# Performance work log

Measured on AMD Instinct MI355X. Metric: run time of the kernel, lower is better.

The kernel has to match this reference:

```python
import jax, jax.numpy as jnp
import numpy as np

N, CIN, COUT, K = 16384, 3, 3, 20

def prelu(x, a):
    return jnp.maximum(x, 0) + a * jnp.minimum(x, 0)

def knn_ind(x, k):
    # pairwise squared distances; topk of -d includes self (d=0), matching torch
    xx = jnp.sum(x * x, axis=1, keepdims=True)          # [n,1]
    d = xx + xx.T - 2.0 * (x @ x.T)                      # [n,n]
    return jax.lax.top_k(-d, k)[1]                       # [n,k] int32

def graph_features(x, k):
    ind = knn_ind(x, k)                                  # [n,k]
    xi = x[ind]                                          # [n,k,C] gather
    x_ = jnp.broadcast_to(x[:, None, :], xi.shape)       # [n,k,C]
    return jnp.concatenate([xi - x_, x_], axis=-1)       # [n,k,2C]

def edge_conv(x, k, layers):
    f = graph_features(x, k)                             # [n,k,2C]
    for (W, a) in layers:
        f = prelu(f @ W, a)
    return jnp.max(f, axis=-2)                           # [n,Cout] max over k neighbors

def setup_inputs() -> dict:
    key = jax.random.key(0)
    ks = jax.random.split(key, 16)
    def w(kk, i, o):
        return jax.random.normal(kk, (i, o), jnp.float32) * (1.0 / np.sqrt(i))
    p = jnp.float32(0.25)
    return {
        "x": jax.random.normal(ks[0], (N, CIN), jnp.float32),
        "hidden": jax.random.normal(ks[1], (1,), jnp.float32),
        "W1a": w(ks[2], 2 * CIN, 64), "p1a": p,
        "W1b": w(ks[3], 64, 64),      "p1b": p,
        "W2a": w(ks[4], 128, 64),     "p2a": p,
        "W2b": w(ks[5], 64, 64),      "p2b": p,
        "W3":  w(ks[6], 128, 64),     "p3": p,
        "W4":  w(ks[7], 192, 1024),   "p4": p,
        "W5":  w(ks[8], 1024 + 192, 256), "p5": p,
        "W6":  w(ks[9], 256, 256),    "p6": p,
        "W7":  w(ks[10], 256, 128),   "p7": p,
        "W8":  w(ks[11], 128, COUT),  "p8": p,
    }

def reference(x, hidden, W1a, p1a, W1b, p1b, W2a, p2a, W2b, p2b, W3, p3,
              W4, p4, W5, p5, W6, p6, W7, p7, W8, p8):
    n = x.shape[0]
    x1 = edge_conv(x, K, [(W1a, p1a), (W1b, p1b)])       # [n,64]
    x2 = edge_conv(x1, K, [(W2a, p2a), (W2b, p2b)])      # [n,64]
    x3 = edge_conv(x2, K, [(W3, p3)])                    # [n,64]
    x4 = jnp.concatenate([x1, x2, x3], axis=-1)          # [n,192]
    x5 = prelu(x4 @ W4, p4)                              # [n,1024]
    x5 = jnp.broadcast_to(jnp.max(x5, axis=0, keepdims=True), (n, 1024))
    h = jnp.concatenate([x1, x2, x3, x5], axis=-1)       # [n,1216]
    h = prelu(h @ W5, p5)                                # dropout = identity (eval)
    h = prelu(h @ W6, p6)
    h = prelu(h @ W7, p7)
    h = prelu(h @ W8, p8)                                # [n,COUT]
    return (h, hidden)
```

## Files before the change

kernel.cpp:

```cpp
#include <hip/hip_runtime.h>
#include <hip/hip_bf16.h>
#include <float.h>

#define NPTS 16384
#define KK 20
#define COUT 3
#define SURV_CAP 256
#define RQSLOTS 256

typedef float f4 __attribute__((ext_vector_type(4)));
typedef float f32x4 __attribute__((ext_vector_type(4)));
typedef short bh8 __attribute__((ext_vector_type(8)));

__device__ __forceinline__ void ins20(float (&td)[KK], float &kmax, float nd) {
  float cd = nd;
#pragma unroll
  for (int j = 0; j < KK; ++j) {
    float t0 = td[j];
    bool lt = cd < t0;
    td[j] = lt ? cd : t0;
    cd = lt ? t0 : cd;
  }
  kmax = td[KK - 1];
}

__device__ __forceinline__ void ins4(float (&td)[4], float &kmax, float nd) {
  float cd = nd;
#pragma unroll
  for (int j = 0; j < 4; ++j) {
    float t0 = td[j];
    bool lt = cd < t0;
    td[j] = lt ? cd : t0;
    cd = lt ? t0 : cd;
  }
  kmax = td[3];
}

__device__ __forceinline__ void ins20p(float (&td)[KK], int (&ti)[KK],
                                       float &kmax, float nd, int ni) {
  float cd = nd; int ci = ni;
#pragma unroll
  for (int j = 0; j < KK; ++j) {
    float t0 = td[j]; int t1 = ti[j];
    bool lt = cd < t0;
    td[j] = lt ? cd : t0;  ti[j] = lt ? ci : t1;
    cd = lt ? t0 : cd;     ci = lt ? t1 : ci;
  }
  kmax = td[KK - 1];
}

template<int C>
__global__ void norms_kernel(const float* __restrict__ X, int ldx, float* __restrict__ vn) {
  int i = blockIdx.x * 256 + threadIdx.x;
  if (i >= NPTS) return;
  const float* row = X + (size_t)i * ldx;
  float s = 0.f;
#pragma unroll
  for (int c = 0; c < C; ++c) s = fmaf(row[c], row[c], s);
  vn[i] = s;
}

__global__ __launch_bounds__(256)
void mean64_kernel(const float* __restrict__ X, int ldx, float* __restrict__ mean) {
  __shared__ float p[256];
  const int d = blockIdx.x, t = threadIdx.x;
  float s = 0.f;
  for (int r = t; r < NPTS; r += 256) s += X[(size_t)r * ldx + d];
  p[t] = s;
  __syncthreads();
  for (int o = 128; o > 0; o >>= 1) { if (t < o) p[t] += p[t + o]; __syncthreads(); }
  if (t == 0) mean[d] = p[0] * (1.0f / NPTS);
}

__global__ __launch_bounds__(256)
void xc_kernel(const float* __restrict__ X, int ldx, const float* __restrict__ mean,
               float* __restrict__ Xc, short* __restrict__ Xbf,
               float* __restrict__ vn, float* __restrict__ sn) {
  __shared__ float msh[64];
  const int t = threadIdx.x;
  if (t < 64) msh[t] = mean[t];
  __syncthreads();
  const int row = blockIdx.x * 32 + (t >> 3), sub = t & 7;
  f4 a = *(const f4*)&X[(size_t)row * ldx + sub * 8];
  f4 b = *(const f4*)&X[(size_t)row * ldx + sub * 8 + 4];
#pragma unroll
  for (int e = 0; e < 4; ++e) { a[e] -= msh[sub * 8 + e]; b[e] -= msh[sub * 8 + 4 + e]; }
  *(f4*)&Xc[(size_t)row * 64 + sub * 8] = a;
  *(f4*)&Xc[(size_t)row * 64 + sub * 8 + 4] = b;
  bh8 o;
#pragma unroll
  for (int e = 0; e < 4; ++e) {
    __hip_bfloat16 ha = __float2bfloat16(a[e]);
    __hip_bfloat16 hb = __float2bfloat16(b[e]);
    o[e] = *reinterpret_cast<short*>(&ha);
    o[4 + e] = *reinterpret_cast<short*>(&hb);
  }
  *(bh8*)&Xbf[(size_t)row * 64 + sub * 8] = o;
  float s = a[0]*a[0] + a[1]*a[1] + a[2]*a[2] + a[3]*a[3]
          + b[0]*b[0] + b[1]*b[1] + b[2]*b[2] + b[3]*b[3];
  s += __shfl_xor(s, 1);
  s += __shfl_xor(s, 2);
  s += __shfl_xor(s, 4);
  if (sub == 0) { vn[row] = s; sn[row] = sqrtf(s); }
}

template<int C>
__global__ __launch_bounds__(256, 2)
void sampleTv4_kernel(const float* __restrict__ X, const float* __restrict__ vn,
                      float* __restrict__ plist) {
  __shared__ __align__(16) float Qs[C * 64];
  __shared__ __align__(16) float Cs[C * 132];
  __shared__ float cn[128];
  const int t = threadIdx.x;
  const int qb = blockIdx.x * 64;
  const int tb = blockIdx.y ? 11 : 0;
  const int nt = blockIdx.y ? 10 : 11;

  if constexpr (C == 64) {
#pragma unroll
    for (int u = 0; u < 4; ++u) {
      int idx = u * 256 + t;
      int q = idx & 63, dg = idx >> 6;
      f4 v = *(const f4*)&X[(size_t)(qb + q) * C + dg * 4];
#pragma unroll
      for (int e = 0; e < 4; ++e) Qs[(dg * 4 + e) * 64 + q] = v[e];
    }
  } else {
    for (int idx = t; idx < C * 64; idx += 256) {
      int q = idx & 63, d = idx >> 6;
      Qs[d * 64 + q] = X[(size_t)(qb + q) * C + d];
    }
  }

  const int tq = t & 15, tc = t >> 4;
  const int q0 = tq * 4, c0 = tc * 8;

  float l4[4][4]; float km[4];
#pragma unroll
  for (int i = 0; i < 4; ++i) {
    km[i] = FLT_MAX;
#pragma unroll
    for (int k = 0; k < 4; ++k) l4[i][k] = FLT_MAX;
  }

  for (int tt = 0; tt < nt; ++tt) {
    const int base = (tb + tt) * 128;
    __syncthreads();
    if constexpr (C == 64) {
#pragma unroll
      for (int u = 0; u < 8; ++u) {
        int idx = u * 256 + t;
        int r = idx & 127, dg = idx >> 7;
        f4 v = *(const f4*)&X[(size_t)((base + r) * 6) * C + dg * 4];
#pragma unroll
        for (int e = 0; e < 4; ++e) Cs[(dg * 4 + e) * 132 + r] = v[e];
      }
    } else {
      for (int idx = t; idx < C * 128; idx += 256) {
        int r = idx & 127, d = idx >> 7;
        Cs[d * 132 + r] = X[(size_t)((base + r) * 6) * C + d];
      }
    }
    if (t < 128) cn[t] = vn[(base + t) * 6];
    __syncthreads();

    float acc[4][8];
#pragma unroll
    for (int i = 0; i < 4; ++i)
#pragma unroll
      for (int j = 0; j < 8; ++j) acc[i][j] = 0.f;

#pragma unroll 4
    for (int d = 0; d < C; ++d) {
      f4 qa = *(const f4*)&Qs[d * 64 + q0];
      f4 ca = *(const f4*)&Cs[d * 132 + c0];
      f4 cb = *(const f4*)&Cs[d * 132 + c0 + 4];
      float cr[8] = {ca[0], ca[1], ca[2], ca[3], cb[0], cb[1], cb[2], cb[3]};
#pragma unroll
      for (int i = 0; i < 4; ++i)
#pragma unroll
        for (int j = 0; j < 8; ++j)
          acc[i][j] = fmaf(qa[i], cr[j], acc[i][j]);
    }

#pragma unroll
    for (int j = 0; j < 8; ++j) {
      float cv = cn[c0 + j];
#pragma unroll
      for (int i = 0; i < 4; ++i) {
        float sv = fmaf(-2.f, acc[i][j], cv);
        if (sv < km[i]) ins4(l4[i], km[i], sv);
      }
    }
  }

#pragma unroll
  for (int i = 0; i < 4; ++i) {
    size_t off = (((size_t)blockIdx.y * NPTS + (qb + q0 + i)) * 16 + tc) * 4;
    f4 v = {l4[i][0], l4[i][1], l4[i][2], l4[i][3]};
    *(f4*)&plist[off] = v;
  }
}

__global__ __launch_bounds__(256)
void mergeT_kernel(const float* __restrict__ plist, float* __restrict__ T,
                   unsigned* __restrict__ cnt, unsigned* __restrict__ redoCnt) {
  const int q = blockIdx.x * 256 + threadIdx.x;
  float td[KK];
#pragma unroll
  for (int j = 0; j < KK; ++j) td[j] = FLT_MAX;
  float km = FLT_MAX;
  for (int s = 0; s < 2; ++s) {
    const float* p = &plist[((size_t)s * NPTS + q) * 64];
    for (int z = 0; z < 64; ++z) {
      float v = p[z];
      if (v < km) ins20(td, km, v);
    }
  }
  T[q] = td[KK - 1] + 1e-4f * (fabsf(td[KK - 1]) + 1.0f);
  cnt[q] = 0u;
  if (q == 0) *redoCnt = 0u;
}

__global__ __launch_bounds__(256, 2)
void knn_filter3_kernel(const float* __restrict__ X, const float* __restrict__ vn,
                        const float* __restrict__ T,
                        float* __restrict__ survd, int* __restrict__ survi,
                        unsigned* __restrict__ cnt) {
  constexpr int CAPB = 40;
  __shared__ __align__(16) f4 CsV[512];
  __shared__ float Tsl[128];
  __shared__ unsigned scnt[128];
  __shared__ float sbD[128 * CAPB];
  __shared__ int   sbI[128 * CAPB];

  const int t = threadIdx.x;
  const int qb = blockIdx.x * 128;
  const int cbase = blockIdx.y * 2048;
  if (t < 128) { Tsl[t] = T[qb + t]; scnt[t] = 0u; }
  __syncthreads();

  const int tq = t & 15, tc = t >> 4;
  const int q0 = tq * 8, c0loc = tc * 8;

  float qx[8], qy[8], qz[8], tr[8];
#pragma unroll
  for (int i = 0; i < 8; ++i) {
    const float* qr = &X[(size_t)(qb + q0 + i) * 3];
    qx[i] = qr[0]; qy[i] = qr[1]; qz[i] = qr[2];
    tr[i] = Tsl[q0 + i];
  }

  for (int rd = 0; rd < 4; ++rd) {
    const int cb = cbase + rd * 512;
    __syncthreads();
#pragma unroll
    for (int u = 0; u < 2; ++u) {
      int idx = u * 256 + t;
      int c = cb + idx;
      const float* cr = &X[(size_t)c * 3];
      f4 v = {cr[0], cr[1], cr[2], vn[c]};
      CsV[idx] = v;
    }
    __syncthreads();

#pragma unroll
    for (int sub = 0; sub < 4; ++sub) {
      const int cl0 = sub * 128 + c0loc;
#pragma unroll
      for (int j = 0; j < 8; ++j) {
        f4 cv = CsV[cl0 + j];
        const int cglob = cb + cl0 + j;
#pragma unroll
        for (int i = 0; i < 8; ++i) {
          float d0 = fmaf(qx[i], cv[0], fmaf(qy[i], cv[1], qz[i] * cv[2]));
          float sv = fmaf(-2.f, d0, cv[3]);
          if (sv <= tr[i]) {
            unsigned p = atomicAdd(&scnt[q0 + i], 1u);
            if (p < CAPB) {
              sbD[(q0 + i) * CAPB + p] = sv;
              sbI[(q0 + i) * CAPB + p] = cglob;
            } else {
              unsigned gp = atomicAdd(&cnt[qb + q0 + i], 1u);
              if (gp < SURV_CAP) {
                survd[(size_t)(qb + q0 + i) * SURV_CAP + gp] = sv;
                survi[(size_t)(qb + q0 + i) * SURV_CAP + gp] = cglob;
              }
            }
          }
        }
      }
    }
  }

  __syncthreads();
  if (t < 128) {
    unsigned n = scnt[t]; if (n > CAPB) n = CAPB;
    if (n) {
      unsigned base = atomicAdd(&cnt[qb + t], n);
      for (unsigned i = 0; i < n; ++i) {
        unsigned p = base + i;
        if (p < SURV_CAP) {
          survd[(size_t)(qb + t) * SURV_CAP + p] = sbD[t * CAPB + i];
          survi[(size_t)(qb + t) * SURV_CAP + p] = sbI[t * CAPB + i];
        }
      }
    }
  }
}

__global__ __launch_bounds__(256, 2)
void knn_filter64_mfma(const short* __restrict__ Xbf, const float* __restrict__ vn,
                       const float* __restrict__ sn, const float* __restrict__ T,
                       int* __restrict__ survi, unsigned* __restrict__ cnt) {
  __shared__ __align__(16) short Qs[128 * 64];
  __shared__ __align__(16) short Cs[128 * 64];
  __shared__ float vnc[128], snq[128], snc[128], Tq[128];
  __shared__ unsigned scnt[128];
  __shared__ int sbI[128 * 8];

  const int t = threadIdx.x;
  const int qb = blockIdx.x * 128, cb = blockIdx.y * 128;

#pragma unroll
  for (int p = 0; p < 4; ++p) {
    int idx = p * 256 + t;
    int row = idx >> 3, sl = idx & 7;
    int slq = sl ^ (row & 7);
    *(bh8*)&Qs[row * 64 + slq * 8] = *(const bh8*)&Xbf[(size_t)(qb + row) * 64 + sl * 8];
    *(bh8*)&Cs[row * 64 + slq * 8] = *(const bh8*)&Xbf[(size_t)(cb + row) * 64 + sl * 8];
  }
  if (t < 128) { Tq[t] = T[qb + t]; snq[t] = sn[qb + t]; scnt[t] = 0u; }
  else { vnc[t - 128] = vn[cb + t - 128]; snc[t - 128] = sn[cb + t - 128]; }
  __syncthreads();

  const int w = t >> 6, l = t & 63;
  const int qsub = (w >> 1) * 64, csub = (w & 1) * 64;
  const int lr = l & 15, lh = l >> 4;

  f32x4 acc[4][4];
#pragma unroll
  for (int i = 0; i < 4; ++i)
#pragma unroll
    for (int j = 0; j < 4; ++j) acc[i][j] = f32x4{0.f, 0.f, 0.f, 0.f};

#pragma unroll
  for (int kk = 0; kk < 2; ++kk) {
    const int sl = kk * 4 + lh;
    bh8 af[4], bf[4];
#pragma unroll
    for (int i = 0; i < 4; ++i) {
      int qr = qsub + i * 16 + lr;
      af[i] = *(const bh8*)&Qs[qr * 64 + (sl ^ (qr & 7)) * 8];
      int cr = csub + i * 16 + lr;
      bf[i] = *(const bh8*)&Cs[cr * 64 + (sl ^ (cr & 7)) * 8];
    }
#pragma unroll
    for (int i = 0; i < 4; ++i)
#pragma unroll
      for (int j = 0; j < 4; ++j)
        acc[i][j] = __builtin_amdgcn_mfma_f32_16x16x32_bf16(af[i], bf[j], acc[i][j], 0, 0, 0);
  }

#pragma unroll
  for (int i = 0; i < 4; ++i) {
#pragma unroll
    for (int r = 0; r < 4; ++r) {
      const int ql = qsub + i * 16 + lh * 4 + r;
      const float tcut = Tq[ql];
      const float sq = snq[ql];
      const int q = qb + ql;
#pragma unroll
      for (int j = 0; j < 4; ++j) {
        const int cl = csub + j * 16 + lr;
        float s = fmaf(-2.f, acc[i][j][r], vnc[cl]);
        float margin = 0.0082f * sq * snc[cl] + 1e-6f;
        if (s <= tcut + margin) {
          unsigned p = atomicAdd(&scnt[ql], 1u);
          if (p < 8u) sbI[ql * 8 + p] = cb + cl;
          else {
            unsigned gp = atomicAdd(&cnt[q], 1u);
            if (gp < SURV_CAP) survi[(size_t)q * SURV_CAP + gp] = cb + cl;
          }
        }
      }
    }
  }

  __syncthreads();
  if (t < 128) {
    unsigned n = scnt[t]; if (n > 8u) n = 8u;
    if (n) {
      unsigned base = atomicAdd(&cnt[qb + t], n);
      for (unsigned i = 0; i < n; ++i) {
        unsigned p = base + i;
        if (p < SURV_CAP) survi[(size_t)(qb + t) * SURV_CAP + p] = sbI[t * 8 + i];
      }
    }
  }
}

template<int C>
__global__ __launch_bounds__(256, 2)
void exact_kernel(const float* __restrict__ X, int ldx, const float* __restrict__ vn,
                  const unsigned* __restrict__ cnt, const int* __restrict__ survi,
                  float* __restrict__ survd) {
  __shared__ float qsh[C];
  const int q = blockIdx.x;
  const int t = threadIdx.x;
  if (t < C) qsh[t] = X[(size_t)q * ldx + t];
  __syncthreads();
  unsigned n = cnt[q];
  if (n > SURV_CAP) n = SURV_CAP;
  if (t < n) {
    const int c = survi[(size_t)q * SURV_CAP + t];
    const float* crow = X + (size_t)c * ldx;
    float d0 = 0.f, d1 = 0.f, d2 = 0.f, d3 = 0.f;
#pragma unroll
    for (int s = 0; s < C / 4; ++s) {
      f4 cv = *(const f4*)&crow[s * 4];
      d0 = fmaf(cv[0], qsh[s * 4 + 0], d0);
      d1 = fmaf(cv[1], qsh[s * 4 + 1], d1);
      d2 = fmaf(cv[2], qsh[s * 4 + 2], d2);
      d3 = fmaf(cv[3], qsh[s * 4 + 3], d3);
    }
    survd[(size_t)q * SURV_CAP + t] = fmaf(-2.f, (d0 + d1) + (d2 + d3), vn[c]);
  }
}

__global__ __launch_bounds__(256, 2)
void select_kernel(const float* __restrict__ survd, const int* __restrict__ survi,
                   const unsigned* __restrict__ cnt, int* __restrict__ ind,
                   unsigned* __restrict__ redoCnt, int* __restrict__ redoList) {
  const int q = blockIdx.x * 256 + threadIdx.x;
  const unsigned n = cnt[q];
  if (n > SURV_CAP) {
    unsigned p = atomicAdd(redoCnt, 1u);
    redoList[p] = q;
    return;
  }
  float td[KK]; int ti[KK];
#pragma unroll
  for (int j = 0; j < KK; ++j) { td[j] = FLT_MAX; ti[j] = 0; }
  float kmax = FLT_MAX;
  for (unsigned i = 0; i < n; ++i) {
    float d = survd[(size_t)q * SURV_CAP + i];
    if (d < kmax) ins20p(td, ti, kmax, d, survi[(size_t)q * SURV_CAP + i]);
  }
#pragma unroll
  for (int j = 0; j < KK; ++j) ind[q * KK + j] = ti[j];
}

template<int C>
__global__ __launch_bounds__(256, 2)
void knn_redo_p1(const float* __restrict__ X, int ldx, const float* __restrict__ vn,
                 const int* __restrict__ redoList, const unsigned* __restrict__ redoCnt,
                 float* __restrict__ rpd, int* __restrict__ rpi) {
  __shared__ float lds_d[256 * KK];
  __shared__ int   lds_i[256 * KK];
  const int t = threadIdx.x;
  const unsigned n = *redoCnt;
  const unsigned e = blockIdx.x >> 5;
  const int part = blockIdx.x & 31;
  if (e >= n || e >= (unsigned)RQSLOTS) return;
  const int q = redoList[e];
  float qreg[C];
#pragma unroll
  for (int d = 0; d < C; ++d) qreg[d] = X[(size_t)q * ldx + d];
  float td[KK]; int ti[KK];
#pragma unroll
  for (int j = 0; j < KK; ++j) { td[j] = FLT_MAX; ti[j] = 0; }
  float kmax = FLT_MAX;
  const int cbase = part * 512;
#pragma unroll
  for (int u = 0; u < 2; ++u) {
    const int c = cbase + u * 256 + t;
    const float* crow = X + (size_t)c * ldx;
    float d0 = 0.f;
    if constexpr (C >= 4) {
      float d1 = 0.f, d2 = 0.f, d3 = 0.f;
#pragma unroll
      for (int s = 0; s < C / 4; ++s) {
        f4 cv = *(const f4*)&crow[s * 4];
        d0 = fmaf(cv[0], qreg[s * 4 + 0], d0);
        d1 = fmaf(cv[1], qreg[s * 4 + 1], d1);
        d2 = fmaf(cv[2], qreg[s * 4 + 2], d2);
        d3 = fmaf(cv[3], qreg[s * 4 + 3], d3);
      }
      d0 = (d0 + d1) + (d2 + d3);
    } else {
#pragma unroll
      for (int d = 0; d < C; ++d) d0 = fmaf(crow[d], qreg[d], d0);
    }
    float sv = fmaf(-2.f, d0, vn[c]);
    if (sv < kmax) ins20p(td, ti, kmax, sv, c);
  }
#pragma unroll
  for (int j = 0; j < KK; ++j) { lds_d[t * KK + j] = td[j]; lds_i[t * KK + j] = ti[j]; }
  __syncthreads();
#pragma unroll
  for (int G = 1; G <= 64; G *= 4) {
    const int nth = (G == 64) ? 1 : (G == 16) ? 4 : (G == 4) ? 16 : 64;
    if (t < nth) {
      float md[KK]; int mi[KK];
#pragma unroll
      for (int j = 0; j < KK; ++j) { md[j] = FLT_MAX; mi[j] = 0; }
      float km = FLT_MAX;
      for (int s = 0; s < 4; ++s) {
        int base = ((t * 4 + s) * G) * KK;
        for (int j = 0; j < KK; ++j) {
          float v = lds_d[base + j];
          if (v < km) ins20p(md, mi, km, v, lds_i[base + j]);
          else break;
        }
      }
      int obase = (t * 4 * G) * KK;
#pragma unroll
      for (int j = 0; j < KK; ++j) { lds_d[obase + j] = md[j]; lds_i[obase + j] = mi[j]; }
    }
    __syncthreads();
  }
  if (t == 0) {
    size_t off = ((size_t)e * 32 + part) * KK;
#pragma unroll
    for (int j = 0; j < KK; ++j) { rpd[off + j] = lds_d[j]; rpi[off + j] = lds_i[j]; }
  }
}

__global__ __launch_bounds__(256)
void knn_redo_p2(const int* __restrict__ redoList, const unsigned* __restrict__ redoCnt,
                 const float* __restrict__ rpd, const int* __restrict__ rpi,
                 int* __restrict__ ind) {
  const unsigned e = blockIdx.x * 256 + threadIdx.x;
  const unsigned n = *redoCnt;
  if (e >= n || e >= (unsigned)RQSLOTS) return;
  const int q = redoList[e];
  float td[KK]; int ti[KK];
#pragma unroll
  for (int j = 0; j < KK; ++j) { td[j] = FLT_MAX; ti[j] = 0; }
  float kmax = FLT_MAX;
  for (int p = 0; p < 32; ++p) {
    const float* dd = &rpd[((size_t)e * 32 + p) * KK];
    const int* ii = &rpi[((size_t)e * 32 + p) * KK];
    for (int j = 0; j < KK; ++j) {
      float v = dd[j];
      if (v < kmax) ins20p(td, ti, kmax, v, ii[j]);
      else break;
    }
  }
#pragma unroll
  for (int j = 0; j < KK; ++j) ind[q * KK + j] = ti[j];
}

template<int C>
__global__ __launch_bounds__(256, 2)
void knn_redo_kernel(const float* __restrict__ X, int ldx, const float* __restrict__ vn,
                     const int* __restrict__ redoList, const unsigned* __restrict__ redoCnt,
                     int* __restrict__ ind, unsigned ebase) {
  __shared__ float lds_d[256 * KK];
  __shared__ int   lds_i[256 * KK];
  const int t = threadIdx.x;
  const unsigned n = *redoCnt;
  for (unsigned e = ebase + blockIdx.x; e < n; e += gridDim.x) {
    const int q = redoList[e];
    float qreg[C];
#pragma unroll
    for (int d = 0; d < C; ++d) qreg[d] = X[(size_t)q * ldx + d];
    float td[KK]; int ti[KK];
#pragma unroll
    for (int j = 0; j < KK; ++j) { td[j] = FLT_MAX; ti[j] = 0; }
    float kmax = FLT_MAX;
    for (int c = t; c < NPTS; c += 256) {
      const float* crow = X + (size_t)c * ldx;
      float d0 = 0.f;
      if constexpr (C >= 4) {
        float d1 = 0.f, d2 = 0.f, d3 = 0.f;
#pragma unroll
        for (int s = 0; s < C / 4; ++s) {
          f4 cv = *(const f4*)&crow[s * 4];
          d0 = fmaf(cv[0], qreg[s * 4 + 0], d0);
          d1 = fmaf(cv[1], qreg[s * 4 + 1], d1);
          d2 = fmaf(cv[2], qreg[s * 4 + 2], d2);
          d3 = fmaf(cv[3], qreg[s * 4 + 3], d3);
        }
        d0 = (d0 + d1) + (d2 + d3);
      } else {
#pragma unroll
        for (int d = 0; d < C; ++d) d0 = fmaf(crow[d], qreg[d], d0);
      }
      float sv = fmaf(-2.f, d0, vn[c]);
      if (sv < kmax) ins20p(td, ti, kmax, sv, c);
    }
#pragma unroll
    for (int j = 0; j < KK; ++j) { lds_d[t * KK + j] = td[j]; lds_i[t * KK + j] = ti[j]; }
    __syncthreads();
#pragma unroll
    for (int G = 1; G <= 64; G *= 4) {
      const int nth = (G == 64) ? 1 : (G == 16) ? 4 : (G == 4) ? 16 : 64;
      if (t < nth) {
        float md[KK]; int mi[KK];
#pragma unroll
        for (int j = 0; j < KK; ++j) { md[j] = FLT_MAX; mi[j] = 0; }
        float km = FLT_MAX;
        for (int s = 0; s < 4; ++s) {
          int base = ((t * 4 + s) * G) * KK;
          for (int j = 0; j < KK; ++j) {
            float v = lds_d[base + j];
            if (v < km) ins20p(md, mi, km, v, lds_i[base + j]);
            else break;
          }
        }
        int obase = (t * 4 * G) * KK;
#pragma unroll
        for (int j = 0; j < KK; ++j) { lds_d[obase + j] = md[j]; lds_i[obase + j] = mi[j]; }
      }
      __syncthreads();
    }
    if (t == 0) {
#pragma unroll
      for (int j = 0; j < KK; ++j) ind[q * KK + j] = lds_i[j];
    }
    __syncthreads();
  }
}

template<int CIN>
__global__ __launch_bounds__(256, 2)
void ub_kernel(const float* __restrict__ X, int ldx, const float* __restrict__ W1,
               float* __restrict__ UB) {
  __shared__ __align__(16) float Ws[2 * CIN * 64];
  __shared__ __align__(16) float Xs[32][(CIN == 3) ? 4 : CIN];
  const int t = threadIdx.x;
  for (int idx = t; idx < 2 * CIN * 64; idx += 256) Ws[idx] = W1[idx];
  const int pb = blockIdx.x * 32;
  if constexpr (CIN == 64) {
    int r = t >> 3, g = t & 7;
    f4 a = *(const f4*)&X[(size_t)(pb + r) * ldx + g * 8];
    f4 b = *(const f4*)&X[(size_t)(pb + r) * ldx + g * 8 + 4];
    *(f4*)&Xs[r][g * 8] = a;
    *(f4*)&Xs[r][g * 8 + 4] = b;
  } else {
    if (t < 32 * CIN) {
      int r = t / CIN, d = t - r * CIN;
      Xs[r][d] = X[(size_t)(pb + r) * ldx + d];
    }
  }
  __syncthreads();
  const int p = t >> 3, c0 = (t & 7) * 8;
  float u[8], v[8];
#pragma unroll
  for (int e = 0; e < 8; ++e) { u[e] = 0.f; v[e] = 0.f; }
#pragma unroll 4
  for (int k = 0; k < CIN; ++k) {
    float xv = Xs[p][k];
    f4 wt0 = *(const f4*)&Ws[k * 64 + c0];
    f4 wt1 = *(const f4*)&Ws[k * 64 + c0 + 4];
    f4 wb0 = *(const f4*)&Ws[(CIN + k) * 64 + c0];
    f4 wb1 = *(const f4*)&Ws[(CIN + k) * 64 + c0 + 4];
#pragma unroll
    for (int e = 0; e < 4; ++e) {
      u[e]     = fmaf(xv, wt0[e], u[e]);
      u[4 + e] = fmaf(xv, wt1[e], u[4 + e]);
      v[e]     = fmaf(xv, wb0[e], v[e]);
      v[4 + e] = fmaf(xv, wb1[e], v[4 + e]);
    }
  }
  float* o = &UB[(size_t)(pb + p) * 128];
  f4 a0 = {u[0], u[1], u[2], u[3]}, a1 = {u[4], u[5], u[6], u[7]};
  f4 b0 = {v[0] - u[0], v[1] - u[1], v[2] - u[2], v[3] - u[3]};
  f4 b1 = {v[4] - u[4], v[5] - u[5], v[6] - u[6], v[7] - u[7]};
  *(f4*)&o[c0] = a0;       *(f4*)&o[c0 + 4] = a1;
  *(f4*)&o[64 + c0] = b0;  *(f4*)&o[64 + c0 + 4] = b1;
}

__global__ __launch_bounds__(256, 3)
void edgeconv2_kernel(const float* __restrict__ UB, const int* __restrict__ ind,
                      const float* __restrict__ W2, const float* __restrict__ p1p,
                      const float* __restrict__ p2p,
                      float* __restrict__ Y, int ldy) {
  __shared__ __align__(16) float W2s[64 * 64];
  __shared__ __align__(16) float h1[4][64 * 32];
  __shared__ float Bs[4][64];
  __shared__ int nbs[4][KK];
  const int t = threadIdx.x;
  const int w = t >> 6, l = t & 63;
  const float a1 = *p1p, a2 = *p2p;
  const int i = blockIdx.x * 4 + w;
  for (int idx = t; idx < 64 * 64; idx += 256) W2s[idx] = W2[idx];
  if (l < 16) *(f4*)&Bs[w][l * 4] = *(const f4*)&UB[(size_t)i * 128 + 64 + l * 4];
  if (l < KK) nbs[w][l] = ind[i * KK + l];
  __syncthreads();

  {
    const int kslot = l >> 1, ch0 = (l & 1) * 32;
    if (kslot < KK) {
      const int nb = nbs[w][kslot];
      const float* ur = &UB[(size_t)nb * 128 + ch0];
#pragma unroll
      for (int g = 0; g < 8; ++g) {
        f4 uv = *(const f4*)&ur[g * 4];
#pragma unroll
        for (int e = 0; e < 4; ++e) {
          int c = ch0 + g * 4 + e;
          float hv = uv[e] + Bs[w][c];
          hv = fmaxf(hv, 0.f) + a1 * fminf(hv, 0.f);
          h1[w][c * 32 + kslot] = hv;
        }
      }
    } else {
#pragma unroll
      for (int g = 0; g < 32; ++g) h1[w][(ch0 + g) * 32 + kslot] = 0.f;
    }
  }
  __syncthreads();

  const int kg = l >> 3, cg = l & 7;
  const int k0 = kg * 4, c0 = cg * 8;
  float acc[4][8];
#pragma unroll
  for (int a = 0; a < 4; ++a)
#pragma unroll
    for (int b = 0; b < 8; ++b) acc[a][b] = 0.f;
#pragma unroll 4
  for (int c = 0; c < 64; ++c) {
    f4 hv = *(const f4*)&h1[w][c * 32 + k0];
    f4 w0 = *(const f4*)&W2s[c * 64 + c0];
    f4 w1 = *(const f4*)&W2s[c * 64 + c0 + 4];
    float wr[8] = {w0[0], w0[1], w0[2], w0[3], w1[0], w1[1], w1[2], w1[3]};
#pragma unroll
    for (int a = 0; a < 4; ++a)
#pragma unroll
      for (int b = 0; b < 8; ++b)
        acc[a][b] = fmaf(hv[a], wr[b], acc[a][b]);
  }

  float mx[8];
#pragma unroll
  for (int b = 0; b < 8; ++b) mx[b] = -FLT_MAX;
  if (kg < 5) {
#pragma unroll
    for (int a = 0; a < 4; ++a)
#pragma unroll
      for (int b = 0; b < 8; ++b) {
        float v = fmaxf(acc[a][b], 0.f) + a2 * fminf(acc[a][b], 0.f);
        mx[b] = fmaxf(mx[b], v);
      }
  }
#pragma unroll
  for (int b = 0; b < 8; ++b) {
    mx[b] = fmaxf(mx[b], __shfl_xor(mx[b], 8));
    mx[b] = fmaxf(mx[b], __shfl_xor(mx[b], 16));
    mx[b] = fmaxf(mx[b], __shfl_xor(mx[b], 32));
  }
  if (kg == 0) {
    f4 o0 = {mx[0], mx[1], mx[2], mx[3]}, o1 = {mx[4], mx[5], mx[6], mx[7]};
    float* yp = &Y[(size_t)i * ldy + c0];
    *(f4*)yp = o0;
    *(f4*)(yp + 4) = o1;
  }
}

__global__ __launch_bounds__(256, 4)
void edgeconv1_kernel(const float* __restrict__ UB, const int* __restrict__ ind,
                      const float* __restrict__ p1p, float* __restrict__ Y, int ldy) {
  __shared__ int nbs[4][KK];
  __shared__ float Bs[4][64];
  const int t = threadIdx.x;
  const int w = t >> 6, l = t & 63;
  const float a1 = *p1p;
  const int i = blockIdx.x * 4 + w;
  if (l < KK) nbs[w][l] = ind[i * KK + l];
  if (l < 16) *(f4*)&Bs[w][l * 4] = *(const f4*)&UB[(size_t)i * 128 + 64 + l * 4];
  __syncthreads();
  const float b = Bs[w][l];
  float mx = -FLT_MAX;
#pragma unroll 4
  for (int k = 0; k < KK; ++k) {
    float uv = UB[(size_t)nbs[w][k] * 128 + l];
    float hv = uv + b;
    hv = fmaxf(hv, 0.f) + a1 * fminf(hv, 0.f);
    mx = fmaxf(mx, hv);
  }
  Y[(size_t)i * ldy + l] = mx;
}

__device__ __forceinline__ unsigned fenc(float f) {
  unsigned u = __float_as_uint(f);
  return (u & 0x80000000u) ? ~u : (u | 0x80000000u);
}
__device__ __forceinline__ float fdec(unsigned u) {
  return (u & 0x80000000u) ? __uint_as_float(u & 0x7fffffffu) : __uint_as_float(~u);
}

__global__ void initg_kernel(unsigned* __restrict__ g) {
  g[blockIdx.x * 256 + threadIdx.x] = 0x007FFFFFu;
}

template<int MODE>
__global__ __launch_bounds__(256, 2)
void gemm_kernel(const float* __restrict__ A, int lda,
                 const float* __restrict__ W, int ldw,
                 const float* __restrict__ bias,
                 const float* __restrict__ pptr,
                 float* __restrict__ Cm, int ldc, int Ktot,
                 unsigned* __restrict__ gmax) {
  __shared__ __align__(16) float At[16 * 132];
  __shared__ __align__(16) float Ws[16 * 128];
  const int t = threadIdx.x;
  const int rb = blockIdx.x * 128, cbb = blockIdx.y * 128;
  const int r0 = (t & 15) * 8, c0 = (t >> 4) * 8;
  const float aa = *pptr;

  float acc[8][8];
#pragma unroll
  for (int i = 0; i < 8; ++i)
#pragma unroll
    for (int j = 0; j < 8; ++j) acc[i][j] = 0.f;

  const int sr = t >> 1, skh = (t & 1) * 8;
  const int wk = t >> 4, wc = (t & 15) * 8;

  for (int k0 = 0; k0 < Ktot; k0 += 16) {
    __syncthreads();
    {
      const float* ap = &A[(size_t)(rb + sr) * lda + k0 + skh];
      f4 v0 = *(const f4*)ap;
      f4 v1 = *(const f4*)(ap + 4);
#pragma unroll
      for (int e = 0; e < 4; ++e) {
        At[(skh + e) * 132 + sr] = v0[e];
        At[(skh + 4 + e) * 132 + sr] = v1[e];
      }
      const float* wp = &W[(size_t)(k0 + wk) * ldw + cbb + wc];
      *(f4*)&Ws[wk * 128 + wc] = *(const f4*)wp;
      *(f4*)&Ws[wk * 128 + wc + 4] = *(const f4*)(wp + 4);
    }
    __syncthreads();
#pragma unroll 4
    for (int d = 0; d < 16; ++d) {
      f4 qa = *(const f4*)&At[d * 132 + r0];
      f4 qb = *(const f4*)&At[d * 132 + r0 + 4];
      f4 wa = *(const f4*)&Ws[d * 128 + c0];
      f4 wb = *(const f4*)&Ws[d * 128 + c0 + 4];
      float qr[8] = {qa[0], qa[1], qa[2], qa[3], qb[0], qb[1], qb[2], qb[3]};
      float wr[8] = {wa[0], wa[1], wa[2], wa[3], wb[0], wb[1], wb[2], wb[3]};
#pragma unroll
      for (int i = 0; i < 8; ++i)
#pragma unroll
        for (int j = 0; j < 8; ++j)
          acc[i][j] = fmaf(qr[i], wr[j], acc[i][j]);
    }
  }

  float bv[8];
#pragma unroll
  for (int j = 0; j < 8; ++j) bv[j] = (MODE == 2) ? bias[cbb + c0 + j] : 0.f;
#pragma unroll
  for (int i = 0; i < 8; ++i)
#pragma unroll
    for (int j = 0; j < 8; ++j) {
      float v = acc[i][j] + bv[j];
      acc[i][j] = fmaxf(v, 0.f) + aa * fminf(v, 0.f);
    }

  if (MODE == 1) {
    float cmax[8];
#pragma unroll
    for (int j = 0; j < 8; ++j) {
      cmax[j] = acc[0][j];
#pragma unroll
      for (int i = 1; i < 8; ++i) cmax[j] = fmaxf(cmax[j], acc[i][j]);
    }
    __syncthreads();
#pragma unroll
    for (int j = 0; j < 8; ++j) At[(t & 15) * 132 + c0 + j] = cmax[j];
    __syncthreads();
    if (t < 128) {
      float m = At[t];
      for (int rr = 1; rr < 16; ++rr) m = fmaxf(m, At[rr * 132 + t]);
      atomicMax(&gmax[cbb + t], fenc(m));
    }
  } else {
#pragma unroll
    for (int i = 0; i < 8; ++i) {
      f4 s0 = {acc[i][0], acc[i][1], acc[i][2], acc[i][3]};
      f4 s1 = {acc[i][4], acc[i][5], acc[i][6], acc[i][7]};
      float* cp = &Cm[(size_t)(rb + r0 + i) * ldc + cbb + c0];
      *(f4*)cp = s0;
      *(f4*)(cp + 4) = s1;
    }
  }
}

__global__ void bias5_kernel(const unsigned* __restrict__ gmax, const float* __restrict__ W5,
                             float* __restrict__ bias5) {
  __shared__ float gs[1024];
  __shared__ float pm[4 * 256];
  int t = threadIdx.x;
  gs[t] = fdec(gmax[t]);
  __syncthreads();
  int c = t & 255, p = t >> 8;
  float acc = 0.f;
  for (int j = p * 256; j < p * 256 + 256; ++j)
    acc = fmaf(gs[j], W5[(size_t)(192 + j) * 256 + c], acc);
  pm[p * 256 + c] = acc;
  __syncthreads();
  if (t < 256) bias5[t] = pm[t] + pm[256 + t] + pm[512 + t] + pm[768 + t];
}

__global__ __launch_bounds__(256, 2)
void w8_kernel(const float* __restrict__ A, const float* __restrict__ W8,
               const float* __restrict__ pptr, const float* __restrict__ hidden,
               float* __restrict__ out) {
  __shared__ __align__(16) float As[64 * 132];
  __shared__ float W8s[128 * COUT];
  int t = threadIdx.x;
  int rb = blockIdx.x * 64;
  for (int idx = t; idx < 128 * COUT; idx += 256) W8s[idx] = W8[idx];
  for (int idx = t; idx < 64 * 32; idx += 256) {
    int r = idx >> 5, c4 = idx & 31;
    *(f4*)&As[r * 132 + c4 * 4] = *(const f4*)&A[(size_t)(rb + r) * 128 + c4 * 4];
  }
  const float a = *pptr;
  __syncthreads();
  int r = t >> 2, c = t & 3;
  if (c < COUT) {
    float acc = 0.f;
#pragma unroll 8
    for (int j = 0; j < 128; ++j)
      acc = fmaf(As[r * 132 + j], W8s[j * COUT + c], acc);
    float v = fmaxf(acc, 0.f) + a * fminf(acc, 0.f);
    out[(size_t)(rb + r) * COUT + c] = v;
  }
  if (blockIdx.x == 0 && t == 0) out[(size_t)NPTS * COUT] = hidden[0];
}

extern "C" void kernel_launch(void* const* d_in, const int* in_sizes, int n_in,
                              void* d_out, int out_size, void* d_ws, size_t ws_size,
                              hipStream_t stream) {
  (void)in_sizes; (void)n_in; (void)out_size; (void)ws_size;
  const float* x      = (const float*)d_in[0];
  const float* hidden = (const float*)d_in[1];
  const float* W1a = (const float*)d_in[2];
  const float* p1a = (const float*)d_in[3];
  const float* W1b = (const float*)d_in[4];
  const float* p1b = (const float*)d_in[5];
  const float* W2a = (const float*)d_in[6];
  const float* p2a = (const float*)d_in[7];
  const float* W2b = (const float*)d_in[8];
  const float* p2b = (const float*)d_in[9];
  const float* W3  = (const float*)d_in[10];
  const float* p3  = (const float*)d_in[11];
  const float* W4  = (const float*)d_in[12];
  const float* p4  = (const float*)d_in[13];
  const float* W5  = (const float*)d_in[14];
  const float* p5  = (const float*)d_in[15];
  const float* W6  = (const float*)d_in[16];
  const float* p6  = (const float*)d_in[17];
  const float* W7  = (const float*)d_in[18];
  const float* p7  = (const float*)d_in[19];
  const float* W8  = (const float*)d_in[20];
  const float* p8  = (const float*)d_in[21];
  float* out = (float*)d_out;

  char* ws = (char*)d_ws;
  size_t off = 0;
  auto carve = [&](size_t bytes) -> void* {
    void* p = ws + off;
    off = (off + bytes + 255) & ~(size_t)255;
    return p;
  };
  float*    x4    = (float*)   carve((size_t)NPTS * 192 * 4);
  float*    vn    = (float*)   carve((size_t)NPTS * 4);
  float*    sn    = (float*)   carve((size_t)NPTS * 4);
  int*      ind   = (int*)     carve((size_t)NPTS * KK * 4);
  float*    T     = (float*)   carve((size_t)NPTS * 4);
  unsigned* cnt   = (unsigned*)carve((size_t)NPTS * 4);
  unsigned* redoCnt = (unsigned*)carve(256);
  int*      redoList = (int*)  carve((size_t)NPTS * 4);
  float*    rpd   = (float*)   carve((size_t)RQSLOTS * 32 * KK * 4);
  int*      rpi   = (int*)     carve((size_t)RQSLOTS * 32 * KK * 4);
  float*    meanb = (float*)   carve(64 * 4);
  float*    Xc    = (float*)   carve((size_t)NPTS * 64 * 4);
  short*    Xbf   = (short*)   carve((size_t)NPTS * 64 * 2);
  float*    plist = (float*)   carve((size_t)2 * NPTS * 64 * 4);
  unsigned* gmax  = (unsigned*)carve(1024 * 4);
  float*    bias5 = (float*)   carve(256 * 4);
  float*    h5    = (float*)   carve((size_t)NPTS * 256 * 4);
  float*    h6    = (float*)   carve((size_t)NPTS * 256 * 4);
  float* survd = h5;
  int*   survi = (int*)h6;
  float* h7 = x4;
  float* UB = plist;

  norms_kernel<3><<<64, 256, 0, stream>>>(x, 3, vn);
  sampleTv4_kernel<3><<<dim3(256, 2), 256, 0, stream>>>(x, vn, plist);
  mergeT_kernel<<<64, 256, 0, stream>>>(plist, T, cnt, redoCnt);
  knn_filter3_kernel<<<dim3(128, 8), 256, 0, stream>>>(x, vn, T, survd, survi, cnt);
  select_kernel<<<64, 256, 0, stream>>>(survd, survi, cnt, ind, redoCnt, redoList);
  knn_redo_p1<3><<<RQSLOTS * 32, 256, 0, stream>>>(x, 3, vn, redoList, redoCnt, rpd, rpi);
  knn_redo_p2<<<1, 256, 0, stream>>>(redoList, redoCnt, rpd, rpi, ind);
  knn_redo_kernel<3><<<256, 256, 0, stream>>>(x, 3, vn, redoList, redoCnt, ind, RQSLOTS);
  ub_kernel<3><<<512, 256, 0, stream>>>(x, 3, W1a, UB);
  edgeconv2_kernel<<<4096, 256, 0, stream>>>(UB, ind, W1b, p1a, p1b, x4 + 0, 192);

  mean64_kernel<<<64, 256, 0, stream>>>(x4 + 0, 192, meanb);
  xc_kernel<<<512, 256, 0, stream>>>(x4 + 0, 192, meanb, Xc, Xbf, vn, sn);
  sampleTv4_kernel<64><<<dim3(256, 2), 256, 0, stream>>>(Xc, vn, plist);
  mergeT_kernel<<<64, 256, 0, stream>>>(plist, T, cnt, redoCnt);
  knn_filter64_mfma<<<dim3(128, 128), 256, 0, stream>>>(Xbf, vn, sn, T, survi, cnt);
  exact_kernel<64><<<NPTS, 256, 0, stream>>>(Xc, 64, vn, cnt, survi, survd);
  select_kernel<<<64, 256, 0, stream>>>(survd, survi, cnt, ind, redoCnt, redoList);
  knn_redo_p1<64><<<RQSLOTS * 32, 256, 0, stream>>>(Xc, 64, vn, redoList, redoCnt, rpd, rpi);
  knn_redo_p2<<<1, 256, 0, stream>>>(redoList, redoCnt, rpd, rpi, ind);
  knn_redo_kernel<64><<<256, 256, 0, stream>>>(Xc, 64, vn, redoList, redoCnt, ind, RQSLOTS);
  ub_kernel<64><<<512, 256, 0, stream>>>(x4 + 0, 192, W2a, UB);
  edgeconv2_kernel<<<4096, 256, 0, stream>>>(UB, ind, W2b, p2a, p2b, x4 + 64, 192);

  mean64_kernel<<<64, 256, 0, stream>>>(x4 + 64, 192, meanb);
  xc_kernel<<<512, 256, 0, stream>>>(x4 + 64, 192, meanb, Xc, Xbf, vn, sn);
  sampleTv4_kernel<64><<<dim3(256, 2), 256, 0, stream>>>(Xc, vn, plist);
  mergeT_kernel<<<64, 256, 0, stream>>>(plist, T, cnt, redoCnt);
  knn_filter64_mfma<<<dim3(128, 128), 256, 0, stream>>>(Xbf, vn, sn, T, survi, cnt);
  exact_kernel<64><<<NPTS, 256, 0, stream>>>(Xc, 64, vn, cnt, survi, survd);
  select_kernel<<<64, 256, 0, stream>>>(survd, survi, cnt, ind, redoCnt, redoList);
  knn_redo_p1<64><<<RQSLOTS * 32, 256, 0, stream>>>(Xc, 64, vn, redoList, redoCnt, rpd, rpi);
  knn_redo_p2<<<1, 256, 0, stream>>>(redoList, redoCnt, rpd, rpi, ind);
  knn_redo_kernel<64><<<256, 256, 0, stream>>>(Xc, 64, vn, redoList, redoCnt, ind, RQSLOTS);
  ub_kernel<64><<<512, 256, 0, stream>>>(x4 + 64, 192, W3, UB);
  edgeconv1_kernel<<<4096, 256, 0, stream>>>(UB, ind, p3, x4 + 128, 192);

  initg_kernel<<<4, 256, 0, stream>>>(gmax);
  gemm_kernel<1><<<dim3(128, 8), 256, 0, stream>>>(x4, 192, W4, 1024, nullptr, p4, nullptr, 0, 192, gmax);

  bias5_kernel<<<1, 1024, 0, stream>>>(gmax, W5, bias5);

  gemm_kernel<2><<<dim3(128, 2), 256, 0, stream>>>(x4, 192, W5, 256, bias5, p5, h5, 256, 192, nullptr);
  gemm_kernel<0><<<dim3(128, 2), 256, 0, stream>>>(h5, 256, W6, 256, nullptr, p6, h6, 256, 256, nullptr);
  gemm_kernel<0><<<dim3(128, 1), 256, 0, stream>>>(h6, 256, W7, 128, nullptr, p7, h7, 128, 256, nullptr);
  w8_kernel<<<256, 256, 0, stream>>>(h7, W8, p8, hidden, out);
}
```

Baseline: 1.942 ms.

## Use split-bf16 MFMA GEMMs for the W4 and W5 layers

Replaces the FP32 SIMT GEMMs for the 192->1024 (with global max) and 192->256 layers with an MFMA kernel. Activations and transposed weights are first split into bf16 hi/lo pairs, and three bf16 MFMAs per tile emulate near-FP32 precision. The aim is to move the largest dense GEMM onto the matrix cores. The cost is extra split kernels, extra memory traffic, and a small loss of precision from dropping the lo*lo term.

```diff
diff --git a/kernel.cpp b/kernel.cpp
--- a/kernel.cpp
+++ b/kernel.cpp
@@ -794,6 +794,145 @@
 
 __global__ void initg_kernel(unsigned* __restrict__ g) {
   g[blockIdx.x * 256 + threadIdx.x] = 0x007FFFFFu;
+}
+
+__global__ __launch_bounds__(256)
+void splitA_kernel(const float* __restrict__ X, int n8,
+                   short* __restrict__ hi, short* __restrict__ lo) {
+  int idx = blockIdx.x * 256 + threadIdx.x;
+  if (idx >= n8) return;
+  f4 a = *(const f4*)&X[(size_t)idx * 8];
+  f4 b = *(const f4*)&X[(size_t)idx * 8 + 4];
+  bh8 h, w;
+#pragma unroll
+  for (int e = 0; e < 4; ++e) {
+    float v0 = a[e], v1 = b[e];
+    __hip_bfloat16 h0 = __float2bfloat16(v0);
+    __hip_bfloat16 h1 = __float2bfloat16(v1);
+    __hip_bfloat16 l0 = __float2bfloat16(v0 - __bfloat162float(h0));
+    __hip_bfloat16 l1 = __float2bfloat16(v1 - __bfloat162float(h1));
+    h[e] = *reinterpret_cast<short*>(&h0); h[4 + e] = *reinterpret_cast<short*>(&h1);
+    w[e] = *reinterpret_cast<short*>(&l0); w[4 + e] = *reinterpret_cast<short*>(&l1);
+  }
+  *(bh8*)&hi[(size_t)idx * 8] = h;
+  *(bh8*)&lo[(size_t)idx * 8] = w;
+}
+
+__global__ __launch_bounds__(256)
+void splitWt_kernel(const float* __restrict__ W, int ldw, int M, int K,
+                    short* __restrict__ hi, short* __restrict__ lo) {
+  int idx = blockIdx.x * 256 + threadIdx.x;
+  int kg8 = K / 8;
+  if (idx >= M * kg8) return;
+  int c = idx / kg8, kg = idx - c * kg8;
+  bh8 h, w;
+#pragma unroll
+  for (int e = 0; e < 8; ++e) {
+    float v = W[(size_t)(kg * 8 + e) * ldw + c];
+    __hip_bfloat16 hv = __float2bfloat16(v);
+    __hip_bfloat16 lv = __float2bfloat16(v - __bfloat162float(hv));
+    h[e] = *reinterpret_cast<short*>(&hv);
+    w[e] = *reinterpret_cast<short*>(&lv);
+  }
+  *(bh8*)&hi[(size_t)c * K + kg * 8] = h;
+  *(bh8*)&lo[(size_t)c * K + kg * 8] = w;
+}
+
+template<int MODE, int K>
+__global__ __launch_bounds__(256, 2)
+void gemm_mfma_kernel(const short* __restrict__ Ahi, const short* __restrict__ Alo,
+                      const short* __restrict__ Wthi, const short* __restrict__ Wtlo,
+                      const float* __restrict__ bias, const float* __restrict__ pptr,
+                      float* __restrict__ Cm, int ldc, unsigned* __restrict__ gmax) {
+  __shared__ __align__(16) short Ah[128 * 32], Al[128 * 32];
+  __shared__ __align__(16) short Bh[128 * 32], Bl[128 * 32];
+  const int t = threadIdx.x;
+  const int rb = blockIdx.x * 128, cb = blockIdx.y * 128;
+  const float aa = *pptr;
+  const int w = t >> 6, l = t & 63;
+  const int rsub = (w >> 1) * 64, csub = (w & 1) * 64;
+  const int lr = l & 15, lh = l >> 4;
+
+  f32x4 acc[4][4];
+#pragma unroll
+  for (int i = 0; i < 4; ++i)
+#pragma unroll
+    for (int j = 0; j < 4; ++j) acc[i][j] = f32x4{0.f, 0.f, 0.f, 0.f};
+
+  for (int ck = 0; ck < K; ck += 32) {
+    __syncthreads();
+#pragma unroll
+    for (int u = 0; u < 2; ++u) {
+      int idx = u * 256 + t;
+      int row = idx >> 2, s = idx & 3;
+      int ssw = s ^ (row & 3);
+      *(bh8*)&Ah[row * 32 + ssw * 8] = *(const bh8*)&Ahi[(size_t)(rb + row) * K + ck + s * 8];
+      *(bh8*)&Al[row * 32 + ssw * 8] = *(const bh8*)&Alo[(size_t)(rb + row) * K + ck + s * 8];
+      *(bh8*)&Bh[row * 32 + ssw * 8] = *(const bh8*)&Wthi[(size_t)(cb + row) * K + ck + s * 8];
+      *(bh8*)&Bl[row * 32 + ssw * 8] = *(const bh8*)&Wtlo[(size_t)(cb + row) * K + ck + s * 8];
+    }
+    __syncthreads();
+    bh8 ah[4], al[4], bh_[4], bl_[4];
+#pragma unroll
+    for (int i = 0; i < 4; ++i) {
+      int r = rsub + i * 16 + lr;
+      int ssw = lh ^ (r & 3);
+      ah[i] = *(const bh8*)&Ah[r * 32 + ssw * 8];
+      al[i] = *(const bh8*)&Al[r * 32 + ssw * 8];
+      int c = csub + i * 16 + lr;
+      int csw = lh ^ (c & 3);
+      bh_[i] = *(const bh8*)&Bh[c * 32 + csw * 8];
+      bl_[i] = *(const bh8*)&Bl[c * 32 + csw * 8];
+    }
+#pragma unroll
+    for (int i = 0; i < 4; ++i)
+#pragma unroll
+      for (int j = 0; j < 4; ++j) {
+        acc[i][j] = __builtin_amdgcn_mfma_f32_16x16x32_bf16(ah[i], bh_[j], acc[i][j], 0, 0, 0);
+        acc[i][j] = __builtin_amdgcn_mfma_f32_16x16x32_bf16(ah[i], bl_[j], acc[i][j], 0, 0, 0);
+        acc[i][j] = __builtin_amdgcn_mfma_f32_16x16x32_bf16(al[i], bh_[j], acc[i][j], 0, 0, 0);
+      }
+  }
+
+  if (MODE == 1) {
+    float cmax[4];
+#pragma unroll
+    for (int j = 0; j < 4; ++j) cmax[j] = -FLT_MAX;
+#pragma unroll
+    for (int i = 0; i < 4; ++i)
+#pragma unroll
+      for (int r = 0; r < 4; ++r)
+#pragma unroll
+        for (int j = 0; j < 4; ++j) {
+          float v = acc[i][j][r];
+          v = fmaxf(v, 0.f) + aa * fminf(v, 0.f);
+          cmax[j] = fmaxf(cmax[j], v);
+        }
+#pragma unroll
+    for (int j = 0; j < 4; ++j) {
+      cmax[j] = fmaxf(cmax[j], __shfl_xor(cmax[j], 16));
+      cmax[j] = fmaxf(cmax[j], __shfl_xor(cmax[j], 32));
+    }
+    if (l < 16) {
+#pragma unroll
+      for (int j = 0; j < 4; ++j)
+        atomicMax(&gmax[cb + csub + j * 16 + l], fenc(cmax[j]));
+    }
+  } else {
+#pragma unroll
+    for (int i = 0; i < 4; ++i)
+#pragma unroll
+      for (int r = 0; r < 4; ++r) {
+        const int row = rsub + i * 16 + lh * 4 + r;
+#pragma unroll
+        for (int j = 0; j < 4; ++j) {
+          const int col = csub + j * 16 + lr;
+          float v = acc[i][j][r] + bias[cb + col];
+          v = fmaxf(v, 0.f) + aa * fminf(v, 0.f);
+          Cm[(size_t)(rb + row) * ldc + cb + col] = v;
+        }
+      }
+  }
 }
 
 template<int MODE>
@@ -984,6 +1123,12 @@
   float*    Xc    = (float*)   carve((size_t)NPTS * 64 * 4);
   short*    Xbf   = (short*)   carve((size_t)NPTS * 64 * 2);
   float*    plist = (float*)   carve((size_t)2 * NPTS * 64 * 4);
+  short*    Ahi   = (short*)   carve((size_t)NPTS * 192 * 2);
+  short*    Alo   = (short*)   carve((size_t)NPTS * 192 * 2);
+  short*    Wt4h  = (short*)   carve((size_t)1024 * 192 * 2);
+  short*    Wt4l  = (short*)   carve((size_t)1024 * 192 * 2);
+  short*    Wt5h  = (short*)   carve((size_t)256 * 192 * 2);
+  short*    Wt5l  = (short*)   carve((size_t)256 * 192 * 2);
   unsigned* gmax  = (unsigned*)carve(1024 * 4);
   float*    bias5 = (float*)   carve(256 * 4);
   float*    h5    = (float*)   carve((size_t)NPTS * 256 * 4);
@@ -1030,12 +1175,16 @@
   ub_kernel<64><<<512, 256, 0, stream>>>(x4 + 64, 192, W3, UB);
   edgeconv1_kernel<<<4096, 256, 0, stream>>>(UB, ind, p3, x4 + 128, 192);
 
+  splitA_kernel<<<(NPTS * 192 / 8 + 255) / 256, 256, 0, stream>>>(x4, NPTS * 192 / 8, Ahi, Alo);
+  splitWt_kernel<<<(1024 * 24 + 255) / 256, 256, 0, stream>>>(W4, 1024, 1024, 192, Wt4h, Wt4l);
+  splitWt_kernel<<<(256 * 24 + 255) / 256, 256, 0, stream>>>(W5, 256, 256, 192, Wt5h, Wt5l);
+
   initg_kernel<<<4, 256, 0, stream>>>(gmax);
-  gemm_kernel<1><<<dim3(128, 8), 256, 0, stream>>>(x4, 192, W4, 1024, nullptr, p4, nullptr, 0, 192, gmax);
+  gemm_mfma_kernel<1, 192><<<dim3(128, 8), 256, 0, stream>>>(Ahi, Alo, Wt4h, Wt4l, nullptr, p4, nullptr, 0, gmax);
 
   bias5_kernel<<<1, 1024, 0, stream>>>(gmax, W5, bias5);
 
-  gemm_kernel<2><<<dim3(128, 2), 256, 0, stream>>>(x4, 192, W5, 256, bias5, p5, h5, 256, 192, nullptr);
+  gemm_mfma_kernel<2, 192><<<dim3(128, 2), 256, 0, stream>>>(Ahi, Alo, Wt5h, Wt5l, bias5, p5, h5, 256, nullptr);
   gemm_kernel<0><<<dim3(128, 2), 256, 0, stream>>>(h5, 256, W6, 256, nullptr, p6, h6, 256, 256, nullptr);
   gemm_kernel<0><<<dim3(128, 1), 256, 0, stream>>>(h6, 256, W7, 128, nullptr, p7, h7, 128, 256, nullptr);
   w8_kernel<<<256, 256, 0, stream>>>(h7, W8, p8, hidden, out);
```

After: 1.888 ms. -2.8%, faster.
